# Performance work log

Measured on AMD Instinct MI355X. Metric: run time of the kernel, lower is better.

## Reference

```python
import jax, jax.numpy as jnp
import numpy as np
from jax import lax

# Parameter physical bounds, order: smax, k1, k2, kb
MIN_BOUNDS = np.array([10.0, 0.01, 0.001, 0.001], dtype=np.float32)
MAX_BOUNDS = np.array([500.0, 0.9, 0.2, 0.1], dtype=np.float32)

T, B, H = 2048, 32, 64
N_FORCING, N_STATE, N_PARAM, N_FLUX = 2, 2, 4, 4


def setup_inputs() -> dict:
    key = jax.random.key(0)
    k1, k2 = jax.random.split(key)
    # forcings: [T, B, H, 2] -> (P precip, PET potential ET), non-negative
    forcings = jax.random.uniform(k1, (T, B, H, N_FORCING), dtype=jnp.float32)
    # initial states: [B, H, 2], model default is zeros
    states = jnp.zeros((B, H, N_STATE), dtype=jnp.float32)
    # unconstrained params in [0,1): [B, H, 4] (static -> repeated over T)
    parameters = jax.random.uniform(k2, (B, H, N_PARAM), dtype=jnp.float32)
    return {"forcings": forcings, "states": states, "parameters": parameters}


def _core(states_t, forcings_t, params_t):
    # states_t: [B,H,2], forcings_t: [B,H,2], params_t: [B,H,4]
    S1, S2 = states_t[..., 0], states_t[..., 1]
    P, PET = forcings_t[..., 0], forcings_t[..., 1]
    smax, k1, k2, kb = (params_t[..., i] for i in range(4))
    # flux_calculator
    et = PET * jnp.clip(S1 / smax, 0.0, 1.0)
    q1 = k1 * S1
    perc = k2 * S1
    qb = kb * S2
    fluxes = jnp.stack([et, q1, perc, qb], axis=-1)  # [B,H,4]
    # state_updater (mass balance), then clamp_(min=0)
    S1n = S1 + P - et - q1 - perc
    S2n = S2 + perc - qb
    new_states = jnp.maximum(jnp.stack([S1n, S2n], axis=-1), 0.0)  # [B,H,2]
    return fluxes, new_states


def reference(forcings, states, parameters):
    # transform parameters to physical bounds: min + (max-min)*u
    min_b = jnp.asarray(MIN_BOUNDS)
    max_b = jnp.asarray(MAX_BOUNDS)
    phys_params = min_b + (max_b - min_b) * parameters  # [B,H,4] (static)

    def step(carry, f_t):
        fluxes_t, new_states = _core(carry, f_t, phys_params)
        return new_states, (fluxes_t, new_states)

    _, (fluxes_seq, states_seq) = lax.scan(step, states, forcings)
    # fluxes_seq: [T,B,H,4], states_seq: [T,B,H,2]
    return fluxes_seq, states_seq
```

## Files before the change

### kernel.cpp

```cpp
#include <hip/hip_runtime.h>
#include <stdint.h>

#define T_STEPS 2048
#define N_CELLS 2048
#define GCELLS  64
#define NGROUPS (N_CELLS / GCELLS)
#define CH      32
#define NCH     (T_STEPS / CH)
#define BCHUNK  16
#define NCHUNK  (T_STEPS / BCHUNK)
#define FLUX_ELEMS ((size_t)T_STEPS * N_CELLS * 4)

#define AS3 __attribute__((address_space(3)))
#define AS1 __attribute__((address_space(1)))

__device__ __forceinline__ void step_state(float& S1, float& S2,
                                           float P, float PET,
                                           float inv_smax, float a, float b,
                                           float k2) {
    float a_c  = fmaf(-PET, inv_smax, a);
    float PmP  = P - PET;
    float t1   = fmaf(S1, a_c, P);
    float t2   = fmaf(S1, a, PmP);
    float S1n  = fmaxf(fmaxf(t1, t2), 0.0f);
    float perc = k2 * S1;
    S2 = fmaf(S2, b, perc);
    S1 = S1n;
}

__global__ void __launch_bounds__(64) hydro_scan(
    const float* __restrict__ forc,
    const float* __restrict__ init_state,
    const float* __restrict__ params,
    float* __restrict__ out)
{
    __shared__ float4 tile[4][CH * 32];

    const int g    = blockIdx.x;
    const int L    = threadIdx.x;
    const int cell = g * GCELLS + L;

    float2* out_s = (float2*)(out + FLUX_ELEMS);

    const float4* gf4 = (const float4*)forc;
    const size_t lane_off = (size_t)(L >> 5) * 1024 + (size_t)g * 32 + (L & 31);

#define ISSUE_DMA(c_) do {                                                     \
        const float4* gp_ = gf4 + (size_t)(c_) * (CH * 1024) + lane_off;       \
        AS3 char* lp_ = (AS3 char*)(void*)tile[(c_) & 3];                      \
        _Pragma("unroll")                                                      \
        for (int k_ = 0; k_ < 16; ++k_)                                        \
            __builtin_amdgcn_global_load_lds(                                  \
                (AS1 const void*)(gp_ + (size_t)k_ * 2048),                    \
                (AS3 void*)(lp_ + (size_t)k_ * 1024), 16, 0, 0);               \
    } while (0)

    const float4 u = ((const float4*)params)[cell];
    float2 s0 = ((const float2*)init_state)[cell];

    ISSUE_DMA(0); ISSUE_DMA(1); ISSUE_DMA(2);

    const float smax = 10.0f  + 490.0f * u.x;
    const float k1   = 0.01f  + 0.89f  * u.y;
    const float k2   = 0.001f + 0.199f * u.z;
    const float kb   = 0.001f + 0.099f * u.w;
    const float inv_smax = 1.0f / smax;
    const float a = 1.0f - k1 - k2;
    const float b = 1.0f - kb;
    float S1 = s0.x, S2 = s0.y;

    asm volatile("s_waitcnt vmcnt(32)" ::: "memory");
    __builtin_amdgcn_sched_barrier(0);

    float2 buf[2][8];
    {
        const float2* tp0 = (const float2*)tile[0];
        #pragma unroll
        for (int j = 0; j < 8; ++j) buf[0][j] = tp0[j * GCELLS + L];
    }

    for (int c = 0; c < NCH; ++c) {
        const float2* tp  = (const float2*)tile[c & 3];
        const float2* tpn = (const float2*)tile[(c + 1) & 3];

        #pragma unroll
        for (int grp = 0; grp < 4; ++grp) {
            const int cur = grp & 1, nxt = cur ^ 1;

            if (grp < 3) {
                #pragma unroll
                for (int j = 0; j < 8; ++j)
                    buf[nxt][j] = tp[((grp + 1) * 8 + j) * GCELLS + L];
            } else {
                if (c <= NCH - 4) {
                    ISSUE_DMA(c + 3);
                    asm volatile("s_waitcnt vmcnt(32)" ::: "memory");
                } else if (c == NCH - 3) {
                    asm volatile("s_waitcnt vmcnt(16)" ::: "memory");
                } else if (c == NCH - 2) {
                    asm volatile("s_waitcnt vmcnt(0)" ::: "memory");
                }
                __builtin_amdgcn_sched_barrier(0);
                if (c < NCH - 1) {
                    #pragma unroll
                    for (int j = 0; j < 8; ++j)
                        buf[nxt][j] = tpn[j * GCELLS + L];
                }
            }

            #pragma unroll
            for (int j = 0; j < 8; ++j)
                step_state(S1, S2, buf[cur][j].x, buf[cur][j].y,
                           inv_smax, a, b, k2);

            if ((grp & 1) == 1 && !(c == NCH - 1 && grp == 3)) {
                int t = c * CH + grp * 8 + 7;
                out_s[(size_t)t * N_CELLS + cell] = make_float2(S1, S2);
            }
        }
    }
#undef ISSUE_DMA
}

__global__ void __launch_bounds__(256) hydro_expand(
    const float* __restrict__ forc,
    const float* __restrict__ init_state,
    const float* __restrict__ params,
    float* __restrict__ out)
{
    const int blk  = blockIdx.x;
    const int wave = threadIdx.x >> 6;
    const int L    = threadIdx.x & 63;
    const int c    = blk >> 3;
    const int g    = (blk & 7) * 4 + wave;
    const int cell = g * GCELLS + L;
    const int t0   = c * BCHUNK;

    float4* out_f = (float4*)out;
    float2* out_s = (float2*)(out + FLUX_ELEMS);
    const float2* fp = (const float2*)forc;
    size_t idx = (size_t)t0 * N_CELLS + cell;

    float2 fb[BCHUNK];
    #pragma unroll
    for (int j = 0; j < BCHUNK; ++j) fb[j] = fp[idx + (size_t)j * N_CELLS];

    const float4 u = ((const float4*)params)[cell];
    float2 sp = (c == 0) ? ((const float2*)init_state)[cell]
                         : out_s[(size_t)(t0 - 1) * N_CELLS + cell];

    const float smax = 10.0f  + 490.0f * u.x;
    const float k1   = 0.01f  + 0.89f  * u.y;
    const float k2   = 0.001f + 0.199f * u.z;
    const float kb   = 0.001f + 0.099f * u.w;
    const float inv_smax = 1.0f / smax;
    const float a = 1.0f - k1 - k2;
    const float b = 1.0f - kb;
    float S1 = sp.x, S2 = sp.y;

    #pragma unroll
    for (int j = 0; j < BCHUNK; ++j) {
        float P = fb[j].x, PET = fb[j].y;
        float ratio = fminf(S1 * inv_smax, 1.0f);
        float et    = PET * ratio;
        float q1    = k1 * S1;
        float perc  = k2 * S1;
        float qb    = kb * S2;
        float S1s = S1, S2s = S2;
        step_state(S1s, S2s, P, PET, inv_smax, a, b, k2);
        size_t o = idx + (size_t)j * N_CELLS;
        out_f[o] = make_float4(et, q1, perc, qb);
        out_s[o] = make_float2(S1s, S2s);
        S1 = S1s; S2 = S2s;
    }
}

extern "C" void kernel_launch(void* const* d_in, const int* in_sizes, int n_in,
                              void* d_out, int out_size, void* d_ws, size_t ws_size,
                              hipStream_t stream) {
    const float* forc = (const float*)d_in[0];
    const float* st0  = (const float*)d_in[1];
    const float* prm  = (const float*)d_in[2];
    float* out  = (float*)d_out;

    hipLaunchKernelGGL(hydro_scan, dim3(NGROUPS), dim3(GCELLS), 0, stream,
                       forc, st0, prm, out);
    hipLaunchKernelGGL(hydro_expand, dim3(NCHUNK * NGROUPS / 4), dim3(256), 0, stream,
                       forc, st0, prm, out);
}
```

Measured before the change: 191.8 us.

## Fuse scan and expand kernels with progress-flag producer/consumer overlap

Merges the sequential state scan and the parallel flux expansion into one persistent kernel. Wave 0 of the first 32 blocks runs the scan and publishes checkpoint states plus a per-group progress counter. All other waves poll that counter and expand 16-step chunks as soon as their starting state is ready, so expansion overlaps the scan instead of waiting for a second launch. It also rewrites the S2 recurrence through a scaled variable to shorten the scan's dependency chain. It adds polling, atomics and a timeout fallback that recomputes from the start, with a risk of contention or of relying on co-residency of the blocks.

```diff
diff --git a/kernel.cpp b/kernel.cpp
--- a/kernel.cpp
+++ b/kernel.cpp
@@ -4,50 +4,50 @@
 #define T_STEPS 2048
 #define N_CELLS 2048
 #define GCELLS  64
-#define NGROUPS (N_CELLS / GCELLS)
+#define NGROUPS 32
 #define CH      32
 #define NCH     (T_STEPS / CH)
 #define BCHUNK  16
-#define NCHUNK  (T_STEPS / BCHUNK)
+#define NJOBS   ((T_STEPS / BCHUNK) * NGROUPS)
+#define NBLOCKS 256
+#define TPB     256
+#define NEXPW   (NGROUPS * 3 + (NBLOCKS - NGROUPS) * 4)
 #define FLUX_ELEMS ((size_t)T_STEPS * N_CELLS * 4)
 
 #define AS3 __attribute__((address_space(3)))
 #define AS1 __attribute__((address_space(1)))
 
-__device__ __forceinline__ void step_state(float& S1, float& S2,
-                                           float P, float PET,
-                                           float inv_smax, float a, float b,
-                                           float k2) {
-    float a_c  = fmaf(-PET, inv_smax, a);
-    float PmP  = P - PET;
-    float t1   = fmaf(S1, a_c, P);
-    float t2   = fmaf(S1, a, PmP);
-    float S1n  = fmaxf(fmaxf(t1, t2), 0.0f);
-    float perc = k2 * S1;
-    S2 = fmaf(S2, b, perc);
-    S1 = S1n;
+__device__ uint32_t g_prog[NGROUPS];
+
+__global__ void hydro_init() {
+    if (threadIdx.x < NGROUPS)
+        __hip_atomic_store(&g_prog[threadIdx.x], 0u,
+                           __ATOMIC_RELAXED, __HIP_MEMORY_SCOPE_AGENT);
 }
 
-__global__ void __launch_bounds__(64) hydro_scan(
+__global__ void __launch_bounds__(TPB) hydro_fused(
     const float* __restrict__ forc,
     const float* __restrict__ init_state,
     const float* __restrict__ params,
     float* __restrict__ out)
 {
-    __shared__ float4 tile[4][CH * 32];
-
-    const int g    = blockIdx.x;
-    const int L    = threadIdx.x;
-    const int cell = g * GCELLS + L;
+    __shared__ float4 tile[3][CH * 32];
+
+    const int b = blockIdx.x;
+    const int w = threadIdx.x >> 6;
+    const int L = threadIdx.x & 63;
 
     float2* out_s = (float2*)(out + FLUX_ELEMS);
 
-    const float4* gf4 = (const float4*)forc;
-    const size_t lane_off = (size_t)(L >> 5) * 1024 + (size_t)g * 32 + (L & 31);
-
-#define ISSUE_DMA(c_) do {                                                     \
+    if (b < NGROUPS && w == 0) {
+        const int g = b;
+        const int cell = g * GCELLS + L;
+        const float4* gf4 = (const float4*)forc;
+        const size_t lane_off = (size_t)(L >> 5) * 1024 + (size_t)g * 32 + (L & 31);
+
+#define ISSUE_DMA(c_, ti_) do {                                                \
         const float4* gp_ = gf4 + (size_t)(c_) * (CH * 1024) + lane_off;       \
-        AS3 char* lp_ = (AS3 char*)(void*)tile[(c_) & 3];                      \
+        AS3 char* lp_ = (AS3 char*)(void*)tile[ti_];                           \
         _Pragma("unroll")                                                      \
         for (int k_ = 0; k_ < 16; ++k_)                                        \
             __builtin_amdgcn_global_load_lds(                                  \
@@ -55,123 +55,176 @@
                 (AS3 void*)(lp_ + (size_t)k_ * 1024), 16, 0, 0);               \
     } while (0)
 
-    const float4 u = ((const float4*)params)[cell];
-    float2 s0 = ((const float2*)init_state)[cell];
-
-    ISSUE_DMA(0); ISSUE_DMA(1); ISSUE_DMA(2);
-
-    const float smax = 10.0f  + 490.0f * u.x;
-    const float k1   = 0.01f  + 0.89f  * u.y;
-    const float k2   = 0.001f + 0.199f * u.z;
-    const float kb   = 0.001f + 0.099f * u.w;
-    const float inv_smax = 1.0f / smax;
-    const float a = 1.0f - k1 - k2;
-    const float b = 1.0f - kb;
-    float S1 = s0.x, S2 = s0.y;
-
-    asm volatile("s_waitcnt vmcnt(32)" ::: "memory");
-    __builtin_amdgcn_sched_barrier(0);
-
-    float2 buf[2][8];
-    {
-        const float2* tp0 = (const float2*)tile[0];
-        #pragma unroll
-        for (int j = 0; j < 8; ++j) buf[0][j] = tp0[j * GCELLS + L];
-    }
-
-    for (int c = 0; c < NCH; ++c) {
-        const float2* tp  = (const float2*)tile[c & 3];
-        const float2* tpn = (const float2*)tile[(c + 1) & 3];
-
-        #pragma unroll
-        for (int grp = 0; grp < 4; ++grp) {
-            const int cur = grp & 1, nxt = cur ^ 1;
-
-            if (grp < 3) {
-                #pragma unroll
-                for (int j = 0; j < 8; ++j)
-                    buf[nxt][j] = tp[((grp + 1) * 8 + j) * GCELLS + L];
-            } else {
-                if (c <= NCH - 4) {
-                    ISSUE_DMA(c + 3);
-                    asm volatile("s_waitcnt vmcnt(32)" ::: "memory");
-                } else if (c == NCH - 3) {
-                    asm volatile("s_waitcnt vmcnt(16)" ::: "memory");
-                } else if (c == NCH - 2) {
-                    asm volatile("s_waitcnt vmcnt(0)" ::: "memory");
-                }
-                __builtin_amdgcn_sched_barrier(0);
-                if (c < NCH - 1) {
+        const float4 u = ((const float4*)params)[cell];
+        const float2 s0 = ((const float2*)init_state)[cell];
+
+        ISSUE_DMA(0, 0);
+        ISSUE_DMA(1, 1);
+
+        const float smax = 10.0f  + 490.0f * u.x;
+        const float k1   = 0.01f  + 0.89f  * u.y;
+        const float k2   = 0.001f + 0.199f * u.z;
+        const float kb   = 0.001f + 0.099f * u.w;
+        const float inv_smax = 1.0f / smax;
+        const float a  = 1.0f - k1 - k2;
+        const float bb = 1.0f - kb;
+        float S1 = s0.x;
+        float z  = s0.y / k2;
+
+        asm volatile("s_waitcnt vmcnt(16)" ::: "memory");
+        __builtin_amdgcn_sched_barrier(0);
+
+        int ic = 0, in_ = 1, id_ = 2;
+
+        float2 buf[2][8];
+        {
+            const float2* tc0 = (const float2*)tile[0];
+            #pragma unroll
+            for (int j = 0; j < 8; ++j) buf[0][j] = tc0[j * GCELLS + L];
+        }
+
+        for (int c = 0; c < NCH; ++c) {
+            const float2* tc = (const float2*)tile[ic];
+            const float2* tn = (const float2*)tile[in_];
+            #pragma unroll
+            for (int grp = 0; grp < 4; ++grp) {
+                const int cur = grp & 1, nxt = cur ^ 1;
+                if (grp < 3) {
                     #pragma unroll
                     for (int j = 0; j < 8; ++j)
-                        buf[nxt][j] = tpn[j * GCELLS + L];
-                }
-            }
-
-            #pragma unroll
-            for (int j = 0; j < 8; ++j)
-                step_state(S1, S2, buf[cur][j].x, buf[cur][j].y,
-                           inv_smax, a, b, k2);
-
-            if ((grp & 1) == 1 && !(c == NCH - 1 && grp == 3)) {
-                int t = c * CH + grp * 8 + 7;
-                out_s[(size_t)t * N_CELLS + cell] = make_float2(S1, S2);
-            }
+                        buf[nxt][j] = tc[((grp + 1) * 8 + j) * GCELLS + L];
+                } else {
+                    if (c + 2 < NCH)
+                        asm volatile("s_waitcnt vmcnt(16)" ::: "memory");
+                    else
+                        asm volatile("s_waitcnt vmcnt(0)" ::: "memory");
+                    __builtin_amdgcn_sched_barrier(0);
+                    if (c >= 1 && L == 0)
+                        __hip_atomic_store(&g_prog[g], (uint32_t)(2 * c),
+                                           __ATOMIC_RELAXED,
+                                           __HIP_MEMORY_SCOPE_AGENT);
+                    if (c < NCH - 1) {
+                        #pragma unroll
+                        for (int j = 0; j < 8; ++j)
+                            buf[nxt][j] = tn[j * GCELLS + L];
+                    }
+                }
+                #pragma unroll
+                for (int j = 0; j < 8; ++j) {
+                    const float P = buf[cur][j].x, PET = buf[cur][j].y;
+                    const float a_c = fmaf(-PET, inv_smax, a);
+                    const float PmP = P - PET;
+                    const float t1 = fmaf(S1, a_c, P);
+                    const float t2 = fmaf(S1, a, PmP);
+                    z  = fmaf(z, bb, S1);
+                    S1 = fmaxf(fmaxf(t1, t2), 0.0f);
+                }
+                if (grp == 0 && c + 2 < NCH) ISSUE_DMA(c + 2, id_);
+                if (grp == 1) {
+                    const float2 v = make_float2(S1, k2 * z);
+                    __hip_atomic_store(
+                        (unsigned long long*)&out_s[(size_t)(c * CH + 15) * N_CELLS + cell],
+                        __builtin_bit_cast(unsigned long long, v),
+                        __ATOMIC_RELAXED, __HIP_MEMORY_SCOPE_AGENT);
+                }
+            }
+            {
+                const float2 v = make_float2(S1, k2 * z);
+                __hip_atomic_store(
+                    (unsigned long long*)&out_s[(size_t)(c * CH + 31) * N_CELLS + cell],
+                    __builtin_bit_cast(unsigned long long, v),
+                    __ATOMIC_RELAXED, __HIP_MEMORY_SCOPE_AGENT);
+            }
+            const int tmp = ic; ic = in_; in_ = id_; id_ = tmp;
         }
-    }
+        asm volatile("s_waitcnt vmcnt(0)" ::: "memory");
+        if (L == 0)
+            __hip_atomic_store(&g_prog[g], (uint32_t)(2 * NCH),
+                               __ATOMIC_RELAXED, __HIP_MEMORY_SCOPE_AGENT);
 #undef ISSUE_DMA
-}
-
-__global__ void __launch_bounds__(256) hydro_expand(
-    const float* __restrict__ forc,
-    const float* __restrict__ init_state,
-    const float* __restrict__ params,
-    float* __restrict__ out)
-{
-    const int blk  = blockIdx.x;
-    const int wave = threadIdx.x >> 6;
-    const int L    = threadIdx.x & 63;
-    const int c    = blk >> 3;
-    const int g    = (blk & 7) * 4 + wave;
-    const int cell = g * GCELLS + L;
-    const int t0   = c * BCHUNK;
-
-    float4* out_f = (float4*)out;
-    float2* out_s = (float2*)(out + FLUX_ELEMS);
-    const float2* fp = (const float2*)forc;
-    size_t idx = (size_t)t0 * N_CELLS + cell;
-
-    float2 fb[BCHUNK];
-    #pragma unroll
-    for (int j = 0; j < BCHUNK; ++j) fb[j] = fp[idx + (size_t)j * N_CELLS];
-
-    const float4 u = ((const float4*)params)[cell];
-    float2 sp = (c == 0) ? ((const float2*)init_state)[cell]
-                         : out_s[(size_t)(t0 - 1) * N_CELLS + cell];
-
-    const float smax = 10.0f  + 490.0f * u.x;
-    const float k1   = 0.01f  + 0.89f  * u.y;
-    const float k2   = 0.001f + 0.199f * u.z;
-    const float kb   = 0.001f + 0.099f * u.w;
-    const float inv_smax = 1.0f / smax;
-    const float a = 1.0f - k1 - k2;
-    const float b = 1.0f - kb;
-    float S1 = sp.x, S2 = sp.y;
-
-    #pragma unroll
-    for (int j = 0; j < BCHUNK; ++j) {
-        float P = fb[j].x, PET = fb[j].y;
-        float ratio = fminf(S1 * inv_smax, 1.0f);
-        float et    = PET * ratio;
-        float q1    = k1 * S1;
-        float perc  = k2 * S1;
-        float qb    = kb * S2;
-        float S1s = S1, S2s = S2;
-        step_state(S1s, S2s, P, PET, inv_smax, a, b, k2);
-        size_t o = idx + (size_t)j * N_CELLS;
-        out_f[o] = make_float4(et, q1, perc, qb);
-        out_s[o] = make_float2(S1s, S2s);
-        S1 = S1s; S2 = S2s;
+    } else {
+        const int W = (b < NGROUPS) ? (b * 3 + (w - 1))
+                                    : (NGROUPS * 3 + (b - NGROUPS) * 4 + w);
+        const float2* fp2 = (const float2*)forc;
+        float4* out_f = (float4*)out;
+
+        for (int jid = W; jid < NJOBS; jid += NEXPW) {
+            const int c = jid >> 5, g = jid & 31;
+            const int cell = g * GCELLS + L;
+            const int t0 = c * BCHUNK;
+            const size_t idx = (size_t)t0 * N_CELLS + cell;
+
+            float2 fb[BCHUNK];
+            #pragma unroll
+            for (int k = 0; k < BCHUNK; ++k)
+                fb[k] = fp2[idx + (size_t)k * N_CELLS];
+
+            const float4 u = ((const float4*)params)[cell];
+            const float smax = 10.0f  + 490.0f * u.x;
+            const float k1   = 0.01f  + 0.89f  * u.y;
+            const float k2   = 0.001f + 0.199f * u.z;
+            const float kb   = 0.001f + 0.099f * u.w;
+            const float inv_smax = 1.0f / smax;
+            const float a  = 1.0f - k1 - k2;
+            const float bb = 1.0f - kb;
+
+            float S1, S2;
+            bool have = true;
+            if (c == 0) {
+                const float2 sp = ((const float2*)init_state)[cell];
+                S1 = sp.x; S2 = sp.y;
+            } else {
+                uint32_t polls = 0;
+                for (;;) {
+                    uint32_t p = __hip_atomic_load(&g_prog[g], __ATOMIC_RELAXED,
+                                                   __HIP_MEMORY_SCOPE_AGENT);
+                    if ((polls & 255u) == 255u)
+                        p = __hip_atomic_load(&g_prog[g], __ATOMIC_ACQUIRE,
+                                              __HIP_MEMORY_SCOPE_AGENT);
+                    if (p >= (uint32_t)c) break;
+                    if (++polls > 20000u) { have = false; break; }
+                    __builtin_amdgcn_s_sleep(32);
+                }
+                if (have) {
+                    (void)__hip_atomic_load(&g_prog[g], __ATOMIC_ACQUIRE,
+                                            __HIP_MEMORY_SCOPE_AGENT);
+                    const unsigned long long bits = __hip_atomic_load(
+                        (const unsigned long long*)&out_s[(size_t)(t0 - 1) * N_CELLS + cell],
+                        __ATOMIC_RELAXED, __HIP_MEMORY_SCOPE_AGENT);
+                    const float2 sp = __builtin_bit_cast(float2, bits);
+                    S1 = sp.x; S2 = sp.y;
+                } else {
+                    const float2 sp = ((const float2*)init_state)[cell];
+                    S1 = sp.x; S2 = sp.y;
+                    for (int t = 0; t < t0; ++t) {
+                        const float2 f = fp2[(size_t)t * N_CELLS + cell];
+                        const float ratio = fminf(S1 * inv_smax, 1.0f);
+                        const float u1  = fmaf(S1, a, f.x);
+                        const float S1n = fmaxf(fmaf(-f.y, ratio, u1), 0.0f);
+                        const float S2n = fmaf(S2, bb, k2 * S1);
+                        S1 = S1n; S2 = S2n;
+                    }
+                }
+            }
+
+            #pragma unroll
+            for (int k = 0; k < BCHUNK; ++k) {
+                const float P = fb[k].x, PET = fb[k].y;
+                const float ratio = fminf(S1 * inv_smax, 1.0f);
+                const float et   = PET * ratio;
+                const float q1   = k1 * S1;
+                const float perc = k2 * S1;
+                const float qb   = kb * S2;
+                const float u1   = fmaf(S1, a, P);
+                const float S1n  = fmaxf(u1 - et, 0.0f);
+                const float S2n  = fmaf(S2, bb, perc);
+                const size_t o = idx + (size_t)k * N_CELLS;
+                out_f[o] = make_float4(et, q1, perc, qb);
+                if (k < BCHUNK - 1 || !have)
+                    out_s[o] = make_float2(S1n, S2n);
+                S1 = S1n; S2 = S2n;
+            }
+        }
     }
 }
 
@@ -181,10 +234,9 @@
     const float* forc = (const float*)d_in[0];
     const float* st0  = (const float*)d_in[1];
     const float* prm  = (const float*)d_in[2];
-    float* out  = (float*)d_out;
-
-    hipLaunchKernelGGL(hydro_scan, dim3(NGROUPS), dim3(GCELLS), 0, stream,
-                       forc, st0, prm, out);
-    hipLaunchKernelGGL(hydro_expand, dim3(NCHUNK * NGROUPS / 4), dim3(256), 0, stream,
+    float* out = (float*)d_out;
+
+    hipLaunchKernelGGL(hydro_init, dim3(1), dim3(64), 0, stream);
+    hipLaunchKernelGGL(hydro_fused, dim3(NBLOCKS), dim3(TPB), 0, stream,
                        forc, st0, prm, out);
 }
```

Result: slower. 309.5 us (+61.4%).
